# Kernel optimization log

Measured on AMD Instinct MI355X. Metric: run time of the kernel, lower is better.

## Reference

```python
import jax, jax.numpy as jnp
import numpy as np

B, T, D = 4, 2048, 384
MIN_DUR = 8.0
W_SCALE = 0.02  # keeps softplus output < 8 so clamped+rounded durations are exactly 8


def setup_inputs() -> dict:
    key = jax.random.key(0)
    k_x, k_w1, k_w2 = jax.random.split(key, 3)
    x = jax.random.normal(k_x, (B, T, D), dtype=jnp.float32)
    w1 = jax.random.normal(k_w1, (D, D // 2), dtype=jnp.float32) * W_SCALE
    b1 = jnp.zeros((D // 2,), dtype=jnp.float32)
    w2 = jax.random.normal(k_w2, (D // 2, 1), dtype=jnp.float32) * W_SCALE
    b2 = jnp.zeros((1,), dtype=jnp.float32)
    total_length = B * T * int(MIN_DUR)  # == duration_pred.sum() by construction (all durs clamp to 8)
    return {"x": x, "w1": w1, "b1": b1, "w2": w2, "b2": b2, "total_length": total_length}


def reference(x, w1, b1, w2, b2, total_length):
    # 2-layer MLP duration predictor: Linear -> ReLU -> Linear -> Softplus, squeeze(-1)
    h = jax.nn.relu(jnp.einsum("btd,dh->bth", x, w1) + b1)
    duration_pred = jax.nn.softplus(jnp.einsum("bth,ho->bto", h, w2) + b2)[..., 0]  # (B, T)
    # inference path: clamp to min duration then round
    duration_pred = jnp.round(jnp.maximum(duration_pred, MIN_DUR))
    # Original expands using batch-0 durations for all rows (faithful to source).
    dur0 = duration_pred[0].astype(jnp.int32)            # (T,)
    cum = jnp.cumsum(dur0)                               # (T,) end offsets
    pos = jnp.arange(total_length)                       # static output length
    idx = jnp.minimum(jnp.searchsorted(cum, pos, side="right"), x.shape[1] - 1)
    valid = pos < cum[-1]
    # parallel gather replacing the per-timestep slice-assign loop; zeros past total fill
    expanded = jnp.where(valid[None, :, None], x[:, idx, :], jnp.zeros((), x.dtype))
    return expanded, duration_pred
```

## Files before the change

kernel.cpp:

```cpp
#include <hip/hip_runtime.h>
#include <hip/hip_bf16.h>
#include <math.h>

#define BB 4
#define TT 2048
#define DD 384
#define HH 192
#define TOTAL_LEN 65536
#define EXP_ELEMS (BB * TOTAL_LEN * DD)
#define F4_PER_ROW (DD / 4)
#define TOTAL_F4 (BB * TOTAL_LEN * F4_PER_ROW)
#define ROWS_PER_BLK 16

typedef float f32x4 __attribute__((ext_vector_type(4)));

__global__ __launch_bounds__(256) void mlp_dur_kernel(
    const float* __restrict__ x, const float* __restrict__ w1,
    const float* __restrict__ b1, const float* __restrict__ w2,
    const float* __restrict__ b2, float* __restrict__ dur_out,
    int* __restrict__ dur0) {
  __shared__ float xs[ROWS_PER_BLK * DD];
  __shared__ float part[ROWS_PER_BLK * 4];

  const int tid = threadIdx.x;
  const int lane = tid & 63;
  const int wave = tid >> 6;
  const int row0 = blockIdx.x * ROWS_PER_BLK;

  const f32x4* xg = (const f32x4*)(x + (size_t)row0 * DD);
  f32x4* xs4 = (f32x4*)xs;
#pragma unroll
  for (int i = 0; i < 6; ++i) xs4[i * 256 + tid] = xg[i * 256 + tid];
  __syncthreads();

  float acc[ROWS_PER_BLK];
#pragma unroll
  for (int r = 0; r < ROWS_PER_BLK; ++r) acc[r] = 0.f;

  const int j = tid;
  if (j < HH) {
    for (int k = 0; k < DD; k += 4) {
      float w[4];
#pragma unroll
      for (int kk = 0; kk < 4; ++kk) w[kk] = w1[(size_t)(k + kk) * HH + j];
#pragma unroll
      for (int r = 0; r < ROWS_PER_BLK; ++r) {
        const float* xr = xs + r * DD + k;
#pragma unroll
        for (int kk = 0; kk < 4; ++kk) acc[r] = fmaf(xr[kk], w[kk], acc[r]);
      }
    }
  }

  const float b1v = (j < HH) ? b1[j] : 0.f;
  const float w2v = (j < HH) ? w2[j] : 0.f;

#pragma unroll
  for (int r = 0; r < ROWS_PER_BLK; ++r) {
    float s = fmaxf(acc[r] + b1v, 0.f) * w2v;
#pragma unroll
    for (int off = 32; off > 0; off >>= 1) s += __shfl_down(s, off, 64);
    if (lane == 0) part[r * 4 + wave] = s;
  }
  __syncthreads();

  if (tid < ROWS_PER_BLK) {
    const float z = part[tid * 4] + part[tid * 4 + 1] + part[tid * 4 + 2] +
                    part[tid * 4 + 3] + b2[0];
    const float sp = fmaxf(z, 0.f) + log1pf(expf(-fabsf(z)));
    const float dur = rintf(fmaxf(sp, 8.0f));
    const int row = row0 + tid;
    dur_out[row] = dur;
    if (row < TT) dur0[row] = (int)dur;
  }
}

__global__ __launch_bounds__(256) void scan_kernel(const int* __restrict__ dur0,
                                                   int* __restrict__ cum) {
  __shared__ int lds[256];
  const int tid = threadIdx.x;
  const int base = tid * 8;
  int v[8];
  int run = 0;
#pragma unroll
  for (int i = 0; i < 8; ++i) {
    run += dur0[base + i];
    v[i] = run;
  }
  lds[tid] = run;
  __syncthreads();
  for (int off = 1; off < 256; off <<= 1) {
    const int t = (tid >= off) ? lds[tid - off] : 0;
    __syncthreads();
    lds[tid] += t;
    __syncthreads();
  }
  const int excl = lds[tid] - run;
#pragma unroll
  for (int i = 0; i < 8; ++i) cum[base + i] = v[i] + excl;
}

__global__ __launch_bounds__(256) void idx_kernel(const int* __restrict__ cum,
                                                  int* __restrict__ idx_map) {
  const int pos = blockIdx.x * 256 + threadIdx.x;
  const int total = cum[TT - 1];
  int lo = 0, hi = TT - 1;
  while (lo < hi) {
    const int mid = (lo + hi) >> 1;
    if (cum[mid] > pos) hi = mid;
    else lo = mid + 1;
  }
  idx_map[pos] = (pos < total) ? lo : -1;
}

__global__ __launch_bounds__(256) void expand_kernel(
    const f32x4* __restrict__ x4, const int* __restrict__ idx_map,
    f32x4* __restrict__ out4) {
  const unsigned t = blockIdx.x * 256u + threadIdx.x;
  const unsigned row = t / 96u;
  const unsigned col = t - row * 96u;
  const unsigned b = row >> 16;
  const unsigned pos = row & 65535u;
  const int id = idx_map[pos];
  f32x4 v = {0.f, 0.f, 0.f, 0.f};
  if (id >= 0) v = x4[((size_t)b * TT + (unsigned)id) * F4_PER_ROW + col];
  __builtin_nontemporal_store(v, out4 + t);
}

extern "C" void kernel_launch(void* const* d_in, const int* in_sizes, int n_in,
                              void* d_out, int out_size, void* d_ws,
                              size_t ws_size, hipStream_t stream) {
  const float* x = (const float*)d_in[0];
  const float* w1 = (const float*)d_in[1];
  const float* b1 = (const float*)d_in[2];
  const float* w2 = (const float*)d_in[3];
  const float* b2 = (const float*)d_in[4];

  float* out = (float*)d_out;
  float* dur_out = out + (size_t)EXP_ELEMS;

  int* ws = (int*)d_ws;
  int* dur0 = ws;
  int* cum = ws + TT;
  int* idx_map = ws + 2 * TT;

  mlp_dur_kernel<<<512, 256, 0, stream>>>(x, w1, b1, w2, b2, dur_out, dur0);
  scan_kernel<<<1, 256, 0, stream>>>(dur0, cum);
  idx_kernel<<<TOTAL_LEN / 256, 256, 0, stream>>>(cum, idx_map);
  expand_kernel<<<TOTAL_F4 / 256, 256, 0, stream>>>((const f32x4*)x, idx_map,
                                                    (f32x4*)out);
}
```

Before: 452.0 us.

## Retune MLP blocks, scatter index map, and process four vectors per expand thread

The MLP kernel now runs 192 threads per block with 8 rows each, so no threads sit idle, and it reads x from shared memory as float4 vectors. The binary-search index kernel is replaced by a scatter kernel in which each timestep writes its own output positions. The expand kernel now handles four strided float4 elements per thread to cut the block count. The expand kernel writes about 400MB and dominates runtime, so these changes mainly touch its launch overhead and latency hiding. The scatter kernel may also race between the -1 fill and the index writes if cum values change.

```diff
diff --git a/kernel.cpp b/kernel.cpp
--- a/kernel.cpp
+++ b/kernel.cpp
@@ -10,17 +10,17 @@
 #define EXP_ELEMS (BB * TOTAL_LEN * DD)
 #define F4_PER_ROW (DD / 4)
 #define TOTAL_F4 (BB * TOTAL_LEN * F4_PER_ROW)
-#define ROWS_PER_BLK 16
+#define ROWS_PER_BLK 8
 
 typedef float f32x4 __attribute__((ext_vector_type(4)));
 
-__global__ __launch_bounds__(256) void mlp_dur_kernel(
+__global__ __launch_bounds__(192) void mlp_dur_kernel(
     const float* __restrict__ x, const float* __restrict__ w1,
     const float* __restrict__ b1, const float* __restrict__ w2,
     const float* __restrict__ b2, float* __restrict__ dur_out,
     int* __restrict__ dur0) {
   __shared__ float xs[ROWS_PER_BLK * DD];
-  __shared__ float part[ROWS_PER_BLK * 4];
+  __shared__ float part[ROWS_PER_BLK * 3];
 
   const int tid = threadIdx.x;
   const int lane = tid & 63;
@@ -30,7 +30,7 @@
   const f32x4* xg = (const f32x4*)(x + (size_t)row0 * DD);
   f32x4* xs4 = (f32x4*)xs;
 #pragma unroll
-  for (int i = 0; i < 6; ++i) xs4[i * 256 + tid] = xg[i * 256 + tid];
+  for (int i = 0; i < 4; ++i) xs4[i * 192 + tid] = xg[i * 192 + tid];
   __syncthreads();
 
   float acc[ROWS_PER_BLK];
@@ -38,35 +38,32 @@
   for (int r = 0; r < ROWS_PER_BLK; ++r) acc[r] = 0.f;
 
   const int j = tid;
-  if (j < HH) {
-    for (int k = 0; k < DD; k += 4) {
-      float w[4];
+  for (int k = 0; k < DD; k += 4) {
+    float w[4];
 #pragma unroll
-      for (int kk = 0; kk < 4; ++kk) w[kk] = w1[(size_t)(k + kk) * HH + j];
+    for (int kk = 0; kk < 4; ++kk) w[kk] = w1[(size_t)(k + kk) * HH + j];
 #pragma unroll
-      for (int r = 0; r < ROWS_PER_BLK; ++r) {
-        const float* xr = xs + r * DD + k;
+    for (int r = 0; r < ROWS_PER_BLK; ++r) {
+      const f32x4 xv = *(const f32x4*)(xs + r * DD + k);
 #pragma unroll
-        for (int kk = 0; kk < 4; ++kk) acc[r] = fmaf(xr[kk], w[kk], acc[r]);
-      }
+      for (int kk = 0; kk < 4; ++kk) acc[r] = fmaf(xv[kk], w[kk], acc[r]);
     }
   }
 
-  const float b1v = (j < HH) ? b1[j] : 0.f;
-  const float w2v = (j < HH) ? w2[j] : 0.f;
+  const float b1v = b1[j];
+  const float w2v = w2[j];
 
 #pragma unroll
   for (int r = 0; r < ROWS_PER_BLK; ++r) {
     float s = fmaxf(acc[r] + b1v, 0.f) * w2v;
 #pragma unroll
     for (int off = 32; off > 0; off >>= 1) s += __shfl_down(s, off, 64);
-    if (lane == 0) part[r * 4 + wave] = s;
+    if (lane == 0) part[r * 3 + wave] = s;
   }
   __syncthreads();
 
   if (tid < ROWS_PER_BLK) {
-    const float z = part[tid * 4] + part[tid * 4 + 1] + part[tid * 4 + 2] +
-                    part[tid * 4 + 3] + b2[0];
+    const float z = part[tid * 3] + part[tid * 3 + 1] + part[tid * 3 + 2] + b2[0];
     const float sp = fmaxf(z, 0.f) + log1pf(expf(-fabsf(z)));
     const float dur = rintf(fmaxf(sp, 8.0f));
     const int row = row0 + tid;
@@ -100,31 +97,36 @@
   for (int i = 0; i < 8; ++i) cum[base + i] = v[i] + excl;
 }
 
-__global__ __launch_bounds__(256) void idx_kernel(const int* __restrict__ cum,
-                                                  int* __restrict__ idx_map) {
-  const int pos = blockIdx.x * 256 + threadIdx.x;
-  const int total = cum[TT - 1];
-  int lo = 0, hi = TT - 1;
-  while (lo < hi) {
-    const int mid = (lo + hi) >> 1;
-    if (cum[mid] > pos) hi = mid;
-    else lo = mid + 1;
+__global__ __launch_bounds__(256) void idx_scatter_kernel(
+    const int* __restrict__ dur0, const int* __restrict__ cum,
+    int* __restrict__ idx_map) {
+  const int i = blockIdx.x * 256 + threadIdx.x;
+  const int total = min(cum[TT - 1], TOTAL_LEN);
+  if (i >= total) idx_map[i] = -1;
+  if (i < TT) {
+    const int end = min(cum[i], TOTAL_LEN);
+    const int start = min(end, max(cum[i] - dur0[i], 0));
+    for (int p = start; p < end; ++p) idx_map[p] = i;
   }
-  idx_map[pos] = (pos < total) ? lo : -1;
 }
 
+#define EXP_STRIDE (TOTAL_F4 / 4)
 __global__ __launch_bounds__(256) void expand_kernel(
     const f32x4* __restrict__ x4, const int* __restrict__ idx_map,
     f32x4* __restrict__ out4) {
   const unsigned t = blockIdx.x * 256u + threadIdx.x;
-  const unsigned row = t / 96u;
-  const unsigned col = t - row * 96u;
-  const unsigned b = row >> 16;
-  const unsigned pos = row & 65535u;
-  const int id = idx_map[pos];
-  f32x4 v = {0.f, 0.f, 0.f, 0.f};
-  if (id >= 0) v = x4[((size_t)b * TT + (unsigned)id) * F4_PER_ROW + col];
-  __builtin_nontemporal_store(v, out4 + t);
+#pragma unroll
+  for (int i = 0; i < 4; ++i) {
+    const unsigned e = t + (unsigned)i * EXP_STRIDE;
+    const unsigned row = e / 96u;
+    const unsigned col = e - row * 96u;
+    const unsigned b = row >> 16;
+    const unsigned pos = row & 65535u;
+    const int id = idx_map[pos];
+    f32x4 v = {0.f, 0.f, 0.f, 0.f};
+    if (id >= 0) v = x4[((size_t)b * TT + (unsigned)id) * F4_PER_ROW + col];
+    __builtin_nontemporal_store(v, out4 + e);
+  }
 }
 
 extern "C" void kernel_launch(void* const* d_in, const int* in_sizes, int n_in,
@@ -144,9 +146,10 @@
   int* cum = ws + TT;
   int* idx_map = ws + 2 * TT;
 
-  mlp_dur_kernel<<<512, 256, 0, stream>>>(x, w1, b1, w2, b2, dur_out, dur0);
+  mlp_dur_kernel<<<TT * BB / ROWS_PER_BLK, 192, 0, stream>>>(x, w1, b1, w2, b2,
+                                                             dur_out, dur0);
   scan_kernel<<<1, 256, 0, stream>>>(dur0, cum);
-  idx_kernel<<<TOTAL_LEN / 256, 256, 0, stream>>>(cum, idx_map);
-  expand_kernel<<<TOTAL_F4 / 256, 256, 0, stream>>>((const f32x4*)x, idx_map,
-                                                    (f32x4*)out);
+  idx_scatter_kernel<<<TOTAL_LEN / 256, 256, 0, stream>>>(dur0, cum, idx_map);
+  expand_kernel<<<EXP_STRIDE / 256, 256, 0, stream>>>((const f32x4*)x, idx_map,
+                                                      (f32x4*)out);
 }
```

Result: no change. 454.2 us (+0.5%).
